# Kernel tuning notes

Hardware: AMD Instinct MI355X
Metric: run time of the kernel (lower is better)

## Reference

```python
import jax, jax.numpy as jnp
import numpy as np

B, H, NC, CS, D = 4, 16, 64, 64, 64
BASE_LR = 1.0
EPS = 1e-6


def setup_inputs() -> dict:
    key = jax.random.key(0)
    ks = jax.random.split(key, 4)
    xk = jax.random.normal(ks[0], (B, H, NC, CS, D), jnp.float32)
    xv = jax.random.normal(ks[1], (B, H, NC, CS, D), jnp.float32)
    # weights/theta use the module's N(0, 0.02) init scale
    weight = 0.02 * jax.random.normal(ks[2], (H, D, D), jnp.float32)
    bias = jnp.zeros((H, 1, D), jnp.float32)
    gamma = jnp.ones((H, 1, D), jnp.float32)
    beta = jnp.zeros((H, 1, D), jnp.float32)
    theta = 0.02 * jax.random.normal(ks[3], (H, D, 1), jnp.float32)
    theta_bias = jnp.zeros((H, 1, 1), jnp.float32)
    alpha = jnp.zeros((CS,), jnp.float32)
    return dict(xk=xk, xv=xv, weight=weight, bias=bias, gamma=gamma,
                beta=beta, theta=theta, theta_bias=theta_bias, alpha=alpha)


def _ttt(xk, xv, weight, bias, gamma, beta, theta, theta_bias, alpha):
    Bq, Hq, NCq, CSq, Dq = xk.shape
    # TTTDynamicLearningGate: token_idx = clamp(1/arange + alpha, 0)
    token_idx = jnp.maximum(1.0 / jnp.arange(1, CSq + 1, dtype=xk.dtype) + alpha, 0.0)
    token_eta = token_idx[None, None, :, None]  # [1,1,CS,1]
    g = gamma[None]       # [1,H,1,D]
    bt = beta[None]       # [1,H,1,D]
    tb = theta_bias[None]  # [1,H,1,1]
    # detach(): tile slow weights over batch -> fast weights
    W0 = jnp.broadcast_to(weight[None], (Bq, Hq, Dq, Dq))
    b0 = jnp.broadcast_to(bias[None], (Bq, Hq, 1, Dq))

    def step(carry, chunk):
        W, b = carry
        xk_c, xv_c = chunk  # [B,H,CS,D]
        # lr gate: eta = token_eta * (base_lr * sigmoid(x @ theta + b) / head_dim)
        lr = jax.nn.sigmoid(jnp.einsum('bhkc,hcd->bhkd', xk_c, theta) + tb)
        eta = token_eta * (BASE_LR * lr / Dq)  # [B,H,CS,1]
        # forward through fast weights (depth = 1)
        z = xk_c @ W + b
        # multi-head LayerNorm, detailed
        mu = z.mean(-1, keepdims=True)
        var = ((z - mu) ** 2).mean(-1, keepdims=True)
        std = jnp.sqrt(var + EPS)
        x_hat = (z - mu) / std
        y = g * x_hat + bt
        # L2 reconstruction grad through LN (manual backward)
        grad_out = y - (xv_c - xk_c)
        gxh = grad_out * g
        grad_x = (Dq * gxh - gxh.sum(-1, keepdims=True)
                  - x_hat * (gxh * x_hat).sum(-1, keepdims=True)) / (Dq * std)
        # fast-weight delta + step()
        dW = jnp.einsum('bhkd,bhke->bhde', eta * xk_c, grad_x)
        db = (eta * grad_x).sum(-2, keepdims=True)
        Wn, bn = W - dW, b - db
        return (Wn, bn), xk_c @ Wn + bn

    chunks = (jnp.moveaxis(xk, 2, 0), jnp.moveaxis(xv, 2, 0))  # [NC,B,H,CS,D]
    (_, _), outs = jax.lax.scan(step, (W0, b0), chunks)
    return jnp.moveaxis(outs, 0, 2)  # [B,H,NC,CS,D]


def reference(xk, xv, weight, bias, gamma, beta, theta, theta_bias, alpha):
    return _ttt(xk, xv, weight, bias, gamma, beta, theta, theta_bias, alpha)
```

## Files before the change

### kernel.cpp

```cpp
#include <hip/hip_runtime.h>
#include <hip/hip_bf16.h>
#include <math.h>

#define NCC 64
#define CSC 64
#define DC 64
#define S 72
#define EPSF 1e-6f
#define LDS_BYTES 66560

typedef __attribute__((ext_vector_type(8))) short bf16x8;
typedef __attribute__((ext_vector_type(4))) float f32x4;
typedef __attribute__((ext_vector_type(4))) short short4v;
typedef __attribute__((ext_vector_type(2))) short short2v;

static __device__ __forceinline__ short cvt_bf16(float x) {
    union { __hip_bfloat16 b; short s; } u;
    u.b = __float2bfloat16(x);
    return u.s;
}
static __device__ __forceinline__ float bf16_to_f(unsigned hw) {
    union { unsigned u; float f; } v; v.u = hw << 16;
    return v.f;
}

#define DPP_ROR_ADD(v, N)                                                     \
    do {                                                                      \
        union { float f; int i; } _u, _r;                                     \
        _u.f = (v);                                                           \
        _r.i = __builtin_amdgcn_mov_dpp(_u.i, 0x120 + (N), 0xF, 0xF, true);   \
        (v) += _r.f;                                                          \
    } while (0)

static __device__ __forceinline__ float red16(float v) {
    DPP_ROR_ADD(v, 1);
    DPP_ROR_ADD(v, 2);
    DPP_ROR_ADD(v, 4);
    DPP_ROR_ADD(v, 8);
    return v;
}

__global__ __launch_bounds__(512, 1) void ttt_kernel(
    const float* __restrict__ xk, const float* __restrict__ xv,
    const float* __restrict__ weight, const float* __restrict__ bias,
    const float* __restrict__ gamma, const float* __restrict__ beta,
    const float* __restrict__ theta, const float* __restrict__ theta_bias,
    const float* __restrict__ alpha, float* __restrict__ out)
{
    extern __shared__ char sb[];
    auto xs_rm = (short (*)[CSC][S])(sb);
    auto xsT   = (short (*)[DC][S]) (sb + 18432);
    auto gsT   = (short (*)[S])     (sb + 36864);
    auto Gr    = (short (*)[S])     (sb + 46080);
    auto Wtb   = (short (*)[S])     (sb + 55296);
    auto dbp   = (float (*)[DC])    (sb + 64512);

    const int t   = threadIdx.x;
    const int w   = t >> 6;
    const bool lo = (w < 4);
    const int ws  = w & 3;
    const int l   = t & 63;
    const int g   = l >> 4, la = l & 15;
    const int r0  = 16*ws + 4*g;
    const int io  = lo ? 0 : 2;
    const int ts  = 64*ws + l;
    const int bh  = blockIdx.x;
    const int h   = bh & 15;

    const size_t bh_off = (size_t)bh * NCC*CSC*DC;
    const float* xkb = xk + bh_off;
    const float* xvb = xv + bh_off;
    float*       ob  = out + bh_off;

    float gam[4], bet[4], thv[4], bcol[4];
#pragma unroll
    for (int n = 0; n < 4; ++n) {
        gam[n]  = gamma[h*DC + 16*n + la];
        bet[n]  = beta [h*DC + 16*n + la];
        thv[n]  = theta[h*DC + 16*n + la];
        bcol[n] = bias [h*DC + 16*n + la];
    }
    const float tb = theta_bias[h];
    float tokk[2];
#pragma unroll
    for (int ii = 0; ii < 2; ++ii) {
        int r = r0 + io + ii;
        tokk[ii] = fmaxf(1.0f/(float)(r+1) + alpha[r], 0.0f);
    }

    float Wreg[4][4];
    float4 xl[4];
    float xkh[4][4];
    float xvg[2][4];

#pragma unroll
    for (int ii = 0; ii < 2; ++ii)
#pragma unroll
        for (int n = 0; n < 4; ++n)
            xvg[ii][n] = xvb[(r0+io+ii)*DC + 16*n + la];

    if (lo) {
        const float* wg = weight + h*DC*DC;
#pragma unroll
        for (int i = 0; i < 4; ++i)
#pragma unroll
            for (int n = 0; n < 4; ++n)
                Wreg[i][n] = wg[(r0+i)*DC + 16*n + la];
#pragma unroll
        for (int n = 0; n < 4; ++n) {
            short4v sv;
#pragma unroll
            for (int i = 0; i < 4; ++i) sv[i] = cvt_bf16(Wreg[i][n]);
            *(short4v*)&Wtb[16*n + la][r0] = sv;
        }
#pragma unroll
        for (int i4 = 0; i4 < 4; ++i4) xl[i4] = ((const float4*)xkb)[ts + 256*i4];
#pragma unroll
        for (int i = 0; i < 4; ++i)
#pragma unroll
            for (int n = 0; n < 4; ++n)
                xkh[i][n] = xkb[(r0+i)*DC + 16*n + la];
#pragma unroll
        for (int i4 = 0; i4 < 4; ++i4) {
            int f = ts + 256*i4, k = f >> 4, j = f & 15;
            short4v s4;
            s4[0]=cvt_bf16(xl[i4].x); s4[1]=cvt_bf16(xl[i4].y);
            s4[2]=cvt_bf16(xl[i4].z); s4[3]=cvt_bf16(xl[i4].w);
            *(short4v*)&xs_rm[0][k][4*j] = s4;
        }
#pragma unroll
        for (int n = 0; n < 4; ++n) {
            short4v sv;
#pragma unroll
            for (int i = 0; i < 4; ++i) sv[i] = cvt_bf16(xkh[i][n]);
            *(short4v*)&xsT[0][16*n + la][r0] = sv;
        }
    }
    __syncthreads();

    for (int c = 0; c < NCC; ++c) {
        const int cb = c & 1, nb = cb ^ 1;
        const bool pf = (c + 1 < NCC);

        const bf16x8 a0 = *(const bf16x8*)&xs_rm[cb][16*ws + la][8*g];
        const bf16x8 a1 = *(const bf16x8*)&xs_rm[cb][16*ws + la][32 + 8*g];
        f32x4 zt[4];
#pragma unroll
        for (int n = 0; n < 4; ++n) {
            bf16x8 w0 = *(const bf16x8*)&Wtb[16*n + la][8*g];
            bf16x8 w1 = *(const bf16x8*)&Wtb[16*n + la][32 + 8*g];
            f32x4 zz = {0.f,0.f,0.f,0.f};
            zz = __builtin_amdgcn_mfma_f32_16x16x32_bf16(a0, w0, zz, 0,0,0);
            zz = __builtin_amdgcn_mfma_f32_16x16x32_bf16(a1, w1, zz, 0,0,0);
            zt[n] = zz;
        }
        if (!lo) {
#pragma unroll
            for (int n = 0; n < 4; ++n) {
                bf16x8 b0 = *(const bf16x8*)&xs_rm[cb][16*n + la][8*g];
                bf16x8 b1 = *(const bf16x8*)&xs_rm[cb][16*n + la][32 + 8*g];
                f32x4 cc = {0.f,0.f,0.f,0.f};
                cc = __builtin_amdgcn_mfma_f32_16x16x32_bf16(a0, b0, cc, 0,0,0);
                cc = __builtin_amdgcn_mfma_f32_16x16x32_bf16(a1, b1, cc, 0,0,0);
                short4v sg;
#pragma unroll
                for (int i = 0; i < 4; ++i) sg[i] = cvt_bf16(cc[i]);
                *(short4v*)&Gr[16*n + la][r0] = sg;
            }
        }

        float xkq[2][4];
#pragma unroll
        for (int n = 0; n < 4; ++n) {
            unsigned pk = *(const unsigned*)&xsT[cb][16*n + la][r0 + io];
            xkq[0][n] = bf16_to_f(pk & 0xFFFFu);
            xkq[1][n] = bf16_to_f(pk >> 16);
        }

        float xvN[2][4];
        if (pf) {
            const float* xvn = xvb + (c+1)*CSC*DC;
#pragma unroll
            for (int ii = 0; ii < 2; ++ii)
#pragma unroll
                for (int n = 0; n < 4; ++n)
                    xvN[ii][n] = xvn[(r0+io+ii)*DC + 16*n + la];
            if (lo) {
                const float* xkn = xkb + (c+1)*CSC*DC;
#pragma unroll
                for (int i4 = 0; i4 < 4; ++i4) xl[i4] = ((const float4*)xkn)[ts + 256*i4];
#pragma unroll
                for (int i = 0; i < 4; ++i)
#pragma unroll
                    for (int n = 0; n < 4; ++n)
                        xkh[i][n] = xkn[(r0+i)*DC + 16*n + la];
            }
        }

        float zrow[2][4];
        if (lo) {
#pragma unroll
            for (int n = 0; n < 4; ++n) { zrow[0][n] = zt[n][0]; zrow[1][n] = zt[n][1]; }
        } else {
#pragma unroll
            for (int n = 0; n < 4; ++n) { zrow[0][n] = zt[n][2]; zrow[1][n] = zt[n][3]; }
        }

        float gsv[2][4];
#pragma unroll
        for (int ii = 0; ii < 2; ++ii) {
            float z4[4];
#pragma unroll
            for (int n = 0; n < 4; ++n) z4[n] = zrow[ii][n] + bcol[n];
            float szz = red16(z4[0]*z4[0] + z4[1]*z4[1] + z4[2]*z4[2] + z4[3]*z4[3]);
            float sz  = red16(z4[0] + z4[1] + z4[2] + z4[3]);
            float thd = red16(xkq[ii][0]*thv[0] + xkq[ii][1]*thv[1] +
                              xkq[ii][2]*thv[2] + xkq[ii][3]*thv[3]);
            float mu   = sz * (1.0f/DC);
            float var  = szz*(1.0f/DC) - mu*mu;
            float rstd = rsqrtf(var + EPSF);
            float ex   = __expf(-(thd + tb));
            float lr   = __builtin_amdgcn_rcpf(1.0f + ex);
            float eta  = tokk[ii]*lr*(1.0f/DC);
            float xh[4], gxh[4], a1v = 0.f, a2v = 0.f;
#pragma unroll
            for (int n = 0; n < 4; ++n) {
                xh[n] = (z4[n]-mu)*rstd;
                float y  = fmaf(gam[n], xh[n], bet[n]);
                float go = y - xvg[ii][n] + xkq[ii][n];
                gxh[n] = go*gam[n];
                a1v += gxh[n];
                a2v = fmaf(gxh[n], xh[n], a2v);
            }
            float s1 = red16(a1v), s2 = red16(a2v);
            float sc = rstd*(1.0f/DC)*eta;
#pragma unroll
            for (int n = 0; n < 4; ++n)
                gsv[ii][n] = (64.f*gxh[n] - s1 - xh[n]*s2)*sc;
        }
#pragma unroll
        for (int n = 0; n < 4; ++n) {
            short2v sg;
            sg[0] = cvt_bf16(gsv[0][n]);
            sg[1] = cvt_bf16(gsv[1][n]);
            *(short2v*)&gsT[16*n + la][r0 + io] = sg;
        }
        float dbl[4];
#pragma unroll
        for (int n = 0; n < 4; ++n) {
            float dd = gsv[0][n] + gsv[1][n];
            dd += __shfl_xor(dd, 16);
            dd += __shfl_xor(dd, 32);
            dbl[n] = dd;
        }
        if (l < 16) {
            f32x4 dv = {dbl[0], dbl[1], dbl[2], dbl[3]};
            *(f32x4*)&dbp[w][4*la] = dv;
        }
        __syncthreads();

        {
            f32x4 s = *(const f32x4*)&dbp[0][4*la];
#pragma unroll
            for (int p = 1; p < 8; ++p) {
                f32x4 d = *(const f32x4*)&dbp[p][4*la];
#pragma unroll
                for (int n = 0; n < 4; ++n) s[n] += d[n];
            }
#pragma unroll
            for (int n = 0; n < 4; ++n) bcol[n] -= s[n];
        }

        if (lo) {
            const bf16x8 ax0 = *(const bf16x8*)&xsT[cb][16*ws + la][8*g];
            const bf16x8 ax1 = *(const bf16x8*)&xsT[cb][16*ws + la][32 + 8*g];
#pragma unroll
            for (int n = 0; n < 4; ++n) {
                bf16x8 q0 = *(const bf16x8*)&gsT[16*n + la][8*g];
                bf16x8 q1 = *(const bf16x8*)&gsT[16*n + la][32 + 8*g];
                f32x4 dw = {0.f,0.f,0.f,0.f};
                dw = __builtin_amdgcn_mfma_f32_16x16x32_bf16(ax0, q0, dw, 0,0,0);
                dw = __builtin_amdgcn_mfma_f32_16x16x32_bf16(ax1, q1, dw, 0,0,0);
                short4v sw;
#pragma unroll
                for (int i = 0; i < 4; ++i) {
                    Wreg[i][n] -= dw[i];
                    sw[i] = cvt_bf16(Wreg[i][n]);
                }
                *(short4v*)&Wtb[16*n + la][r0] = sw;
            }
            if (pf) {
#pragma unroll
                for (int i4 = 0; i4 < 4; ++i4) {
                    int f = ts + 256*i4, k = f >> 4, j = f & 15;
                    short4v s4;
                    s4[0]=cvt_bf16(xl[i4].x); s4[1]=cvt_bf16(xl[i4].y);
                    s4[2]=cvt_bf16(xl[i4].z); s4[3]=cvt_bf16(xl[i4].w);
                    *(short4v*)&xs_rm[nb][k][4*j] = s4;
                }
#pragma unroll
                for (int n = 0; n < 4; ++n) {
                    short4v sv;
#pragma unroll
                    for (int i = 0; i < 4; ++i) sv[i] = cvt_bf16(xkh[i][n]);
                    *(short4v*)&xsT[nb][16*n + la][r0] = sv;
                }
            }
        } else {
            const bf16x8 ar0 = *(const bf16x8*)&Gr[16*ws + la][8*g];
            const bf16x8 ar1 = *(const bf16x8*)&Gr[16*ws + la][32 + 8*g];
            float* oc = ob + c*CSC*DC;
#pragma unroll
            for (int n = 0; n < 4; ++n) {
                bf16x8 q0 = *(const bf16x8*)&gsT[16*n + la][8*g];
                bf16x8 q1 = *(const bf16x8*)&gsT[16*n + la][32 + 8*g];
                f32x4 og = {0.f,0.f,0.f,0.f};
                og = __builtin_amdgcn_mfma_f32_16x16x32_bf16(ar0, q0, og, 0,0,0);
                og = __builtin_amdgcn_mfma_f32_16x16x32_bf16(ar1, q1, og, 0,0,0);
#pragma unroll
                for (int i = 0; i < 4; ++i)
                    oc[(r0+i)*DC + 16*n + la] = zt[n][i] - og[i] + bcol[n];
            }
        }
        if (pf) {
#pragma unroll
            for (int ii = 0; ii < 2; ++ii)
#pragma unroll
                for (int n = 0; n < 4; ++n)
                    xvg[ii][n] = xvN[ii][n];
        }
        __syncthreads();
    }
}

extern "C" void kernel_launch(void* const* d_in, const int* in_sizes, int n_in,
                              void* d_out, int out_size, void* d_ws, size_t ws_size,
                              hipStream_t stream) {
    const float* xk         = (const float*)d_in[0];
    const float* xv         = (const float*)d_in[1];
    const float* weight     = (const float*)d_in[2];
    const float* bias       = (const float*)d_in[3];
    const float* gamma      = (const float*)d_in[4];
    const float* beta       = (const float*)d_in[5];
    const float* theta      = (const float*)d_in[6];
    const float* theta_bias = (const float*)d_in[7];
    const float* alpha      = (const float*)d_in[8];
    float* out = (float*)d_out;

    (void)hipFuncSetAttribute((const void*)ttt_kernel,
                              hipFuncAttributeMaxDynamicSharedMemorySize,
                              LDS_BYTES);
    ttt_kernel<<<64, 512, LDS_BYTES, stream>>>(xk, xv, weight, bias, gamma, beta,
                                               theta, theta_bias, alpha, out);
}
```

Baseline: 145.7 us.

## Split TTT chunk work between wave groups and use 32x32 MFMA tiles

Restructures the per-chunk work split. The low waves now own the full LayerNorm backward for their 16 rows, the weight update and the prefetch. The high waves compute the z forward and the Gram matrix with 32x32x16 MFMA and write the output, so the two groups no longer both run the z MFMA and the LN math. The bias correction is folded into Gr as +1 and the high waves carry their own bias column, which shrinks dbp to four entries and drops the xsT readback. This aims to cut duplicated work and MFMA instruction count, at the cost of more load imbalance between the two wave groups and higher register use on the low waves.

```diff
diff --git a/kernel.cpp b/kernel.cpp
--- a/kernel.cpp
+++ b/kernel.cpp
@@ -7,21 +7,17 @@
 #define DC 64
 #define S 72
 #define EPSF 1e-6f
-#define LDS_BYTES 66560
-
-typedef __attribute__((ext_vector_type(8))) short bf16x8;
-typedef __attribute__((ext_vector_type(4))) float f32x4;
-typedef __attribute__((ext_vector_type(4))) short short4v;
-typedef __attribute__((ext_vector_type(2))) short short2v;
+#define LDS_BYTES 65536
+
+typedef __attribute__((ext_vector_type(8)))  short bf16x8;
+typedef __attribute__((ext_vector_type(4)))  float f32x4;
+typedef __attribute__((ext_vector_type(16))) float f32x16;
+typedef __attribute__((ext_vector_type(4)))  short short4v;
 
 static __device__ __forceinline__ short cvt_bf16(float x) {
     union { __hip_bfloat16 b; short s; } u;
     u.b = __float2bfloat16(x);
     return u.s;
-}
-static __device__ __forceinline__ float bf16_to_f(unsigned hw) {
-    union { unsigned u; float f; } v; v.u = hw << 16;
-    return v.f;
 }
 
 #define DPP_ROR_ADD(v, N)                                                     \
@@ -61,8 +57,9 @@
     const int ws  = w & 3;
     const int l   = t & 63;
     const int g   = l >> 4, la = l & 15;
+    const int la5 = l & 31, hi5 = l >> 5;
+    const int R   = ws >> 1, E = ws & 1;
     const int r0  = 16*ws + 4*g;
-    const int io  = lo ? 0 : 2;
     const int ts  = 64*ws + l;
     const int bh  = blockIdx.x;
     const int h   = bh & 15;
@@ -72,54 +69,46 @@
     const float* xvb = xv + bh_off;
     float*       ob  = out + bh_off;
 
-    float gam[4], bet[4], thv[4], bcol[4];
-#pragma unroll
-    for (int n = 0; n < 4; ++n) {
-        gam[n]  = gamma[h*DC + 16*n + la];
-        bet[n]  = beta [h*DC + 16*n + la];
-        thv[n]  = theta[h*DC + 16*n + la];
-        bcol[n] = bias [h*DC + 16*n + la];
-    }
-    const float tb = theta_bias[h];
-    float tokk[2];
-#pragma unroll
-    for (int ii = 0; ii < 2; ++ii) {
-        int r = r0 + io + ii;
-        tokk[ii] = fmaxf(1.0f/(float)(r+1) + alpha[r], 0.0f);
-    }
-
-    float Wreg[4][4];
+    float gam[4], bet[4], thv[4], tok[4], bcol[4], tb = 0.f;
+    float Wreg[16];
     float4 xl[4];
-    float xkh[4][4];
-    float xvg[2][4];
-
-#pragma unroll
-    for (int ii = 0; ii < 2; ++ii)
-#pragma unroll
-        for (int n = 0; n < 4; ++n)
-            xvg[ii][n] = xvb[(r0+io+ii)*DC + 16*n + la];
+    float xkh[4][4], xkE[4][4], xvg[4][4], xvN[4][4];
+    float bcolh = 0.f;
+    f32x16 z32;
 
     if (lo) {
+#pragma unroll
+        for (int n = 0; n < 4; ++n) {
+            gam[n]  = gamma[h*DC + 16*n + la];
+            bet[n]  = beta [h*DC + 16*n + la];
+            thv[n]  = theta[h*DC + 16*n + la];
+            bcol[n] = bias [h*DC + 16*n + la];
+        }
+        tb = theta_bias[h];
+#pragma unroll
+        for (int i = 0; i < 4; ++i)
+            tok[i] = fmaxf(1.0f/(float)(r0+i+1) + alpha[r0+i], 0.0f);
         const float* wg = weight + h*DC*DC;
 #pragma unroll
+        for (int q = 0; q < 4; ++q) {
+            short4v sw;
+#pragma unroll
+            for (int j = 0; j < 4; ++j) {
+                Wreg[4*q+j] = wg[(32*R + 8*q + 4*hi5 + j)*DC + 32*E + la5];
+                sw[j] = cvt_bf16(Wreg[4*q+j]);
+            }
+            *(short4v*)&Wtb[32*E + la5][32*R + 8*q + 4*hi5] = sw;
+        }
+#pragma unroll
+        for (int i4 = 0; i4 < 4; ++i4) xl[i4] = ((const float4*)xkb)[ts + 256*i4];
+#pragma unroll
         for (int i = 0; i < 4; ++i)
 #pragma unroll
-            for (int n = 0; n < 4; ++n)
-                Wreg[i][n] = wg[(r0+i)*DC + 16*n + la];
-#pragma unroll
-        for (int n = 0; n < 4; ++n) {
-            short4v sv;
-#pragma unroll
-            for (int i = 0; i < 4; ++i) sv[i] = cvt_bf16(Wreg[i][n]);
-            *(short4v*)&Wtb[16*n + la][r0] = sv;
-        }
-#pragma unroll
-        for (int i4 = 0; i4 < 4; ++i4) xl[i4] = ((const float4*)xkb)[ts + 256*i4];
-#pragma unroll
-        for (int i = 0; i < 4; ++i)
-#pragma unroll
-            for (int n = 0; n < 4; ++n)
+            for (int n = 0; n < 4; ++n) {
                 xkh[i][n] = xkb[(r0+i)*DC + 16*n + la];
+                xvg[i][n] = xvb[(r0+i)*DC + 16*n + la];
+                xkE[i][n] = xkh[i][n];
+            }
 #pragma unroll
         for (int i4 = 0; i4 < 4; ++i4) {
             int f = ts + 256*i4, k = f >> 4, j = f & 15;
@@ -135,6 +124,8 @@
             for (int i = 0; i < 4; ++i) sv[i] = cvt_bf16(xkh[i][n]);
             *(short4v*)&xsT[0][16*n + la][r0] = sv;
         }
+    } else {
+        bcolh = bias[h*DC + 32*E + la5];
     }
     __syncthreads();
 
@@ -142,152 +133,141 @@
         const int cb = c & 1, nb = cb ^ 1;
         const bool pf = (c + 1 < NCC);
 
-        const bf16x8 a0 = *(const bf16x8*)&xs_rm[cb][16*ws + la][8*g];
-        const bf16x8 a1 = *(const bf16x8*)&xs_rm[cb][16*ws + la][32 + 8*g];
-        f32x4 zt[4];
-#pragma unroll
-        for (int n = 0; n < 4; ++n) {
-            bf16x8 w0 = *(const bf16x8*)&Wtb[16*n + la][8*g];
-            bf16x8 w1 = *(const bf16x8*)&Wtb[16*n + la][32 + 8*g];
-            f32x4 zz = {0.f,0.f,0.f,0.f};
-            zz = __builtin_amdgcn_mfma_f32_16x16x32_bf16(a0, w0, zz, 0,0,0);
-            zz = __builtin_amdgcn_mfma_f32_16x16x32_bf16(a1, w1, zz, 0,0,0);
-            zt[n] = zz;
-        }
-        if (!lo) {
+        if (lo) {
+            const bf16x8 a0 = *(const bf16x8*)&xs_rm[cb][16*ws + la][8*g];
+            const bf16x8 a1 = *(const bf16x8*)&xs_rm[cb][16*ws + la][32 + 8*g];
+            f32x4 zt[4];
 #pragma unroll
             for (int n = 0; n < 4; ++n) {
-                bf16x8 b0 = *(const bf16x8*)&xs_rm[cb][16*n + la][8*g];
-                bf16x8 b1 = *(const bf16x8*)&xs_rm[cb][16*n + la][32 + 8*g];
-                f32x4 cc = {0.f,0.f,0.f,0.f};
-                cc = __builtin_amdgcn_mfma_f32_16x16x32_bf16(a0, b0, cc, 0,0,0);
-                cc = __builtin_amdgcn_mfma_f32_16x16x32_bf16(a1, b1, cc, 0,0,0);
+                bf16x8 w0 = *(const bf16x8*)&Wtb[16*n + la][8*g];
+                bf16x8 w1 = *(const bf16x8*)&Wtb[16*n + la][32 + 8*g];
+                f32x4 zz = {0.f,0.f,0.f,0.f};
+                zz = __builtin_amdgcn_mfma_f32_16x16x32_bf16(a0, w0, zz, 0,0,0);
+                zz = __builtin_amdgcn_mfma_f32_16x16x32_bf16(a1, w1, zz, 0,0,0);
+                zt[n] = zz;
+            }
+            if (pf) {
+                const float* xkn = xkb + (c+1)*CSC*DC;
+                const float* xvn = xvb + (c+1)*CSC*DC;
+#pragma unroll
+                for (int i4 = 0; i4 < 4; ++i4) xl[i4] = ((const float4*)xkn)[ts + 256*i4];
+#pragma unroll
+                for (int i = 0; i < 4; ++i)
+#pragma unroll
+                    for (int n = 0; n < 4; ++n) {
+                        xkh[i][n] = xkn[(r0+i)*DC + 16*n + la];
+                        xvN[i][n] = xvn[(r0+i)*DC + 16*n + la];
+                    }
+            }
+            float gsv[4][4];
+#pragma unroll
+            for (int i = 0; i < 4; ++i) {
+                float z0 = zt[0][i]+bcol[0], z1 = zt[1][i]+bcol[1];
+                float z2 = zt[2][i]+bcol[2], z3 = zt[3][i]+bcol[3];
+                float szz = red16(z0*z0 + z1*z1 + z2*z2 + z3*z3);
+                float sz  = red16(z0 + z1 + z2 + z3);
+                float thd = red16(xkE[i][0]*thv[0] + xkE[i][1]*thv[1] +
+                                  xkE[i][2]*thv[2] + xkE[i][3]*thv[3]);
+                float mu   = sz * (1.0f/DC);
+                float var  = szz*(1.0f/DC) - mu*mu;
+                float rstd = rsqrtf(var + EPSF);
+                float ex   = __expf(-(thd + tb));
+                float lr   = __builtin_amdgcn_rcpf(1.0f + ex);
+                float eta  = tok[i]*lr*(1.0f/DC);
+                float zz4[4] = {z0,z1,z2,z3};
+                float xh[4], gxh[4], a1v = 0.f, a2v = 0.f;
+#pragma unroll
+                for (int n = 0; n < 4; ++n) {
+                    xh[n] = (zz4[n]-mu)*rstd;
+                    float y  = fmaf(gam[n], xh[n], bet[n]);
+                    float go = y - xvg[i][n] + xkE[i][n];
+                    gxh[n] = go*gam[n];
+                    a1v += gxh[n];
+                    a2v = fmaf(gxh[n], xh[n], a2v);
+                }
+                float s1 = red16(a1v), s2 = red16(a2v);
+                float sc = rstd*(1.0f/DC)*eta;
+#pragma unroll
+                for (int n = 0; n < 4; ++n)
+                    gsv[i][n] = (64.f*gxh[n] - s1 - xh[n]*s2)*sc;
+            }
+#pragma unroll
+            for (int n = 0; n < 4; ++n) {
                 short4v sg;
 #pragma unroll
-                for (int i = 0; i < 4; ++i) sg[i] = cvt_bf16(cc[i]);
-                *(short4v*)&Gr[16*n + la][r0] = sg;
-            }
-        }
-
-        float xkq[2][4];
-#pragma unroll
-        for (int n = 0; n < 4; ++n) {
-            unsigned pk = *(const unsigned*)&xsT[cb][16*n + la][r0 + io];
-            xkq[0][n] = bf16_to_f(pk & 0xFFFFu);
-            xkq[1][n] = bf16_to_f(pk >> 16);
-        }
-
-        float xvN[2][4];
-        if (pf) {
-            const float* xvn = xvb + (c+1)*CSC*DC;
-#pragma unroll
-            for (int ii = 0; ii < 2; ++ii)
-#pragma unroll
-                for (int n = 0; n < 4; ++n)
-                    xvN[ii][n] = xvn[(r0+io+ii)*DC + 16*n + la];
-            if (lo) {
-                const float* xkn = xkb + (c+1)*CSC*DC;
-#pragma unroll
-                for (int i4 = 0; i4 < 4; ++i4) xl[i4] = ((const float4*)xkn)[ts + 256*i4];
-#pragma unroll
-                for (int i = 0; i < 4; ++i)
-#pragma unroll
-                    for (int n = 0; n < 4; ++n)
-                        xkh[i][n] = xkn[(r0+i)*DC + 16*n + la];
-            }
-        }
-
-        float zrow[2][4];
+                for (int i = 0; i < 4; ++i) sg[i] = cvt_bf16(gsv[i][n]);
+                *(short4v*)&gsT[16*n + la][r0] = sg;
+            }
+            float dbl[4];
+#pragma unroll
+            for (int n = 0; n < 4; ++n) {
+                float dd = gsv[0][n]+gsv[1][n]+gsv[2][n]+gsv[3][n];
+                dd += __shfl_xor(dd, 16);
+                dd += __shfl_xor(dd, 32);
+                dbl[n] = dd;
+            }
+            if (l < 16) {
+                f32x4 dv = {dbl[0], dbl[1], dbl[2], dbl[3]};
+                *(f32x4*)&dbp[ws][4*la] = dv;
+            }
+        } else {
+            bf16x8 az[4], bz[4];
+#pragma unroll
+            for (int s = 0; s < 4; ++s) {
+                az[s] = *(const bf16x8*)&xs_rm[cb][32*R + la5][16*s + 8*hi5];
+                bz[s] = *(const bf16x8*)&Wtb[32*E + la5][16*s + 8*hi5];
+            }
+            f32x16 zz = {0.f,0.f,0.f,0.f,0.f,0.f,0.f,0.f,
+                         0.f,0.f,0.f,0.f,0.f,0.f,0.f,0.f};
+#pragma unroll
+            for (int s = 0; s < 4; ++s)
+                zz = __builtin_amdgcn_mfma_f32_32x32x16_bf16(az[s], bz[s], zz, 0,0,0);
+            z32 = zz;
+            bf16x8 bg[4];
+            if (R == E) {
+#pragma unroll
+                for (int s = 0; s < 4; ++s) bg[s] = az[s];
+            } else {
+#pragma unroll
+                for (int s = 0; s < 4; ++s)
+                    bg[s] = *(const bf16x8*)&xs_rm[cb][32*E + la5][16*s + 8*hi5];
+            }
+            f32x16 gg = {0.f,0.f,0.f,0.f,0.f,0.f,0.f,0.f,
+                         0.f,0.f,0.f,0.f,0.f,0.f,0.f,0.f};
+#pragma unroll
+            for (int s = 0; s < 4; ++s)
+                gg = __builtin_amdgcn_mfma_f32_32x32x16_bf16(az[s], bg[s], gg, 0,0,0);
+#pragma unroll
+            for (int q = 0; q < 4; ++q) {
+                short4v sg;
+#pragma unroll
+                for (int j = 0; j < 4; ++j) sg[j] = cvt_bf16(gg[4*q+j] + 1.0f);
+                *(short4v*)&Gr[32*E + la5][32*R + 8*q + 4*hi5] = sg;
+            }
+        }
+        __syncthreads();
+
         if (lo) {
-#pragma unroll
-            for (int n = 0; n < 4; ++n) { zrow[0][n] = zt[n][0]; zrow[1][n] = zt[n][1]; }
-        } else {
-#pragma unroll
-            for (int n = 0; n < 4; ++n) { zrow[0][n] = zt[n][2]; zrow[1][n] = zt[n][3]; }
-        }
-
-        float gsv[2][4];
-#pragma unroll
-        for (int ii = 0; ii < 2; ++ii) {
-            float z4[4];
-#pragma unroll
-            for (int n = 0; n < 4; ++n) z4[n] = zrow[ii][n] + bcol[n];
-            float szz = red16(z4[0]*z4[0] + z4[1]*z4[1] + z4[2]*z4[2] + z4[3]*z4[3]);
-            float sz  = red16(z4[0] + z4[1] + z4[2] + z4[3]);
-            float thd = red16(xkq[ii][0]*thv[0] + xkq[ii][1]*thv[1] +
-                              xkq[ii][2]*thv[2] + xkq[ii][3]*thv[3]);
-            float mu   = sz * (1.0f/DC);
-            float var  = szz*(1.0f/DC) - mu*mu;
-            float rstd = rsqrtf(var + EPSF);
-            float ex   = __expf(-(thd + tb));
-            float lr   = __builtin_amdgcn_rcpf(1.0f + ex);
-            float eta  = tokk[ii]*lr*(1.0f/DC);
-            float xh[4], gxh[4], a1v = 0.f, a2v = 0.f;
-#pragma unroll
-            for (int n = 0; n < 4; ++n) {
-                xh[n] = (z4[n]-mu)*rstd;
-                float y  = fmaf(gam[n], xh[n], bet[n]);
-                float go = y - xvg[ii][n] + xkq[ii][n];
-                gxh[n] = go*gam[n];
-                a1v += gxh[n];
-                a2v = fmaf(gxh[n], xh[n], a2v);
-            }
-            float s1 = red16(a1v), s2 = red16(a2v);
-            float sc = rstd*(1.0f/DC)*eta;
-#pragma unroll
-            for (int n = 0; n < 4; ++n)
-                gsv[ii][n] = (64.f*gxh[n] - s1 - xh[n]*s2)*sc;
-        }
-#pragma unroll
-        for (int n = 0; n < 4; ++n) {
-            short2v sg;
-            sg[0] = cvt_bf16(gsv[0][n]);
-            sg[1] = cvt_bf16(gsv[1][n]);
-            *(short2v*)&gsT[16*n + la][r0 + io] = sg;
-        }
-        float dbl[4];
-#pragma unroll
-        for (int n = 0; n < 4; ++n) {
-            float dd = gsv[0][n] + gsv[1][n];
-            dd += __shfl_xor(dd, 16);
-            dd += __shfl_xor(dd, 32);
-            dbl[n] = dd;
-        }
-        if (l < 16) {
-            f32x4 dv = {dbl[0], dbl[1], dbl[2], dbl[3]};
-            *(f32x4*)&dbp[w][4*la] = dv;
-        }
-        __syncthreads();
-
-        {
-            f32x4 s = *(const f32x4*)&dbp[0][4*la];
-#pragma unroll
-            for (int p = 1; p < 8; ++p) {
-                f32x4 d = *(const f32x4*)&dbp[p][4*la];
-#pragma unroll
-                for (int n = 0; n < 4; ++n) s[n] += d[n];
-            }
-#pragma unroll
-            for (int n = 0; n < 4; ++n) bcol[n] -= s[n];
-        }
-
-        if (lo) {
-            const bf16x8 ax0 = *(const bf16x8*)&xsT[cb][16*ws + la][8*g];
-            const bf16x8 ax1 = *(const bf16x8*)&xsT[cb][16*ws + la][32 + 8*g];
-#pragma unroll
-            for (int n = 0; n < 4; ++n) {
-                bf16x8 q0 = *(const bf16x8*)&gsT[16*n + la][8*g];
-                bf16x8 q1 = *(const bf16x8*)&gsT[16*n + la][32 + 8*g];
-                f32x4 dw = {0.f,0.f,0.f,0.f};
-                dw = __builtin_amdgcn_mfma_f32_16x16x32_bf16(ax0, q0, dw, 0,0,0);
-                dw = __builtin_amdgcn_mfma_f32_16x16x32_bf16(ax1, q1, dw, 0,0,0);
+            bf16x8 ax[4], bx[4];
+#pragma unroll
+            for (int s = 0; s < 4; ++s) {
+                ax[s] = *(const bf16x8*)&xsT[cb][32*R + la5][16*s + 8*hi5];
+                bx[s] = *(const bf16x8*)&gsT[32*E + la5][16*s + 8*hi5];
+            }
+            f32x16 dw = {0.f,0.f,0.f,0.f,0.f,0.f,0.f,0.f,
+                         0.f,0.f,0.f,0.f,0.f,0.f,0.f,0.f};
+#pragma unroll
+            for (int s = 0; s < 4; ++s)
+                dw = __builtin_amdgcn_mfma_f32_32x32x16_bf16(ax[s], bx[s], dw, 0,0,0);
+#pragma unroll
+            for (int q = 0; q < 4; ++q) {
                 short4v sw;
 #pragma unroll
-                for (int i = 0; i < 4; ++i) {
-                    Wreg[i][n] -= dw[i];
-                    sw[i] = cvt_bf16(Wreg[i][n]);
-                }
-                *(short4v*)&Wtb[16*n + la][r0] = sw;
+                for (int j = 0; j < 4; ++j) {
+                    Wreg[4*q+j] -= dw[4*q+j];
+                    sw[j] = cvt_bf16(Wreg[4*q+j]);
+                }
+                *(short4v*)&Wtb[32*E + la5][32*R + 8*q + 4*hi5] = sw;
             }
             if (pf) {
 #pragma unroll
@@ -305,29 +285,54 @@
                     for (int i = 0; i < 4; ++i) sv[i] = cvt_bf16(xkh[i][n]);
                     *(short4v*)&xsT[nb][16*n + la][r0] = sv;
                 }
+#pragma unroll
+                for (int i = 0; i < 4; ++i)
+#pragma unroll
+                    for (int n = 0; n < 4; ++n) {
+                        xkE[i][n] = xkh[i][n];
+                        xvg[i][n] = xvN[i][n];
+                    }
+            }
+            {
+                f32x4 s = *(const f32x4*)&dbp[0][4*la];
+#pragma unroll
+                for (int p = 1; p < 4; ++p) {
+                    f32x4 d = *(const f32x4*)&dbp[p][4*la];
+#pragma unroll
+                    for (int n = 0; n < 4; ++n) s[n] += d[n];
+                }
+#pragma unroll
+                for (int n = 0; n < 4; ++n) bcol[n] -= s[n];
             }
         } else {
-            const bf16x8 ar0 = *(const bf16x8*)&Gr[16*ws + la][8*g];
-            const bf16x8 ar1 = *(const bf16x8*)&Gr[16*ws + la][32 + 8*g];
+            bf16x8 ag[4], bq[4];
+#pragma unroll
+            for (int s = 0; s < 4; ++s) {
+                ag[s] = *(const bf16x8*)&Gr[32*R + la5][16*s + 8*hi5];
+                bq[s] = *(const bf16x8*)&gsT[32*E + la5][16*s + 8*hi5];
+            }
+            f32x16 og = {0.f,0.f,0.f,0.f,0.f,0.f,0.f,0.f,
+                         0.f,0.f,0.f,0.f,0.f,0.f,0.f,0.f};
+#pragma unroll
+            for (int s = 0; s < 4; ++s)
+                og = __builtin_amdgcn_mfma_f32_32x32x16_bf16(ag[s], bq[s], og, 0,0,0);
             float* oc = ob + c*CSC*DC;
 #pragma unroll
-            for (int n = 0; n < 4; ++n) {
-                bf16x8 q0 = *(const bf16x8*)&gsT[16*n + la][8*g];
-                bf16x8 q1 = *(const bf16x8*)&gsT[16*n + la][32 + 8*g];
-                f32x4 og = {0.f,0.f,0.f,0.f};
-                og = __builtin_amdgcn_mfma_f32_16x16x32_bf16(ar0, q0, og, 0,0,0);
-                og = __builtin_amdgcn_mfma_f32_16x16x32_bf16(ar1, q1, og, 0,0,0);
-#pragma unroll
-                for (int i = 0; i < 4; ++i)
-                    oc[(r0+i)*DC + 16*n + la] = zt[n][i] - og[i] + bcol[n];
-            }
-        }
-        if (pf) {
-#pragma unroll
-            for (int ii = 0; ii < 2; ++ii)
-#pragma unroll
-                for (int n = 0; n < 4; ++n)
-                    xvg[ii][n] = xvN[ii][n];
+            for (int q = 0; q < 4; ++q)
+#pragma unroll
+                for (int j = 0; j < 4; ++j) {
+                    int r = 4*q + j;
+                    oc[(32*R + 8*q + 4*hi5 + j)*DC + 32*E + la5] =
+                        z32[r] - og[r] + bcolh;
+                }
+            {
+                int idx = 4*(la5 & 15) + 2*E + (la5 >> 4);
+                float s0 = dbp[0][idx];
+                s0 += dbp[1][idx];
+                s0 += dbp[2][idx];
+                s0 += dbp[3][idx];
+                bcolh -= s0;
+            }
         }
         __syncthreads();
     }
```

After: 157.7 us. +8.2%, slower.

## Stage chunk outputs in LDS for coalesced deferred stores; fold bias delta into Gram matmul

Applied to the files above, without the earlier changes.

Each chunk's output tile is now written transposed into an LDS buffer. All eight waves store it to global memory with float4 writes at the start of the next iteration, and the last chunk is flushed after the loop. This replaces the scattered per-lane scalar stores and lets the write overlap the next chunk's compute. The bias is kept in LDS and updated by a single wave. The bias-gradient term is folded into the output matmul by adding 1 to the bf16 Gram entries, which removes the per-thread reduction over all waves. This costs extra LDS, an added sync dependency on the output buffer, and a small precision change from rounding G+1 to bf16.

```diff
diff --git a/kernel.cpp b/kernel.cpp
--- a/kernel.cpp
+++ b/kernel.cpp
@@ -6,8 +6,9 @@
 #define CSC 64
 #define DC 64
 #define S 72
+#define SO 68
 #define EPSF 1e-6f
-#define LDS_BYTES 66560
+#define LDS_BYTES 84224
 
 typedef __attribute__((ext_vector_type(8))) short bf16x8;
 typedef __attribute__((ext_vector_type(4))) float f32x4;
@@ -54,6 +55,8 @@
     auto Gr    = (short (*)[S])     (sb + 46080);
     auto Wtb   = (short (*)[S])     (sb + 55296);
     auto dbp   = (float (*)[DC])    (sb + 64512);
+    auto outb  = (float (*)[SO])    (sb + 66560);
+    auto bs    = (float*)           (sb + 83968);
 
     const int t   = threadIdx.x;
     const int w   = t >> 6;
@@ -72,13 +75,12 @@
     const float* xvb = xv + bh_off;
     float*       ob  = out + bh_off;
 
-    float gam[4], bet[4], thv[4], bcol[4];
+    float gam[4], bet[4], thv[4];
 #pragma unroll
     for (int n = 0; n < 4; ++n) {
-        gam[n]  = gamma[h*DC + 16*n + la];
-        bet[n]  = beta [h*DC + 16*n + la];
-        thv[n]  = theta[h*DC + 16*n + la];
-        bcol[n] = bias [h*DC + 16*n + la];
+        gam[n] = gamma[h*DC + 16*n + la];
+        bet[n] = beta [h*DC + 16*n + la];
+        thv[n] = theta[h*DC + 16*n + la];
     }
     const float tb = theta_bias[h];
     float tokk[2];
@@ -87,6 +89,8 @@
         int r = r0 + io + ii;
         tokk[ii] = fmaxf(1.0f/(float)(r+1) + alpha[r], 0.0f);
     }
+
+    if (t < DC) bs[t] = bias[h*DC + 16*(t & 3) + (t >> 2)];
 
     float Wreg[4][4];
     float4 xl[4];
@@ -141,6 +145,21 @@
     for (int c = 0; c < NCC; ++c) {
         const int cb = c & 1, nb = cb ^ 1;
         const bool pf = (c + 1 < NCC);
+
+        f32x4 bold = *(const f32x4*)&bs[4*la];
+        if (c > 0) {
+            float* ocp = ob + (c-1)*CSC*DC;
+            const int kk = 4*w + (l >> 4);
+            const int e0 = 4*(l & 15);
+#pragma unroll
+            for (int p = 0; p < 2; ++p) {
+                int k2 = kk + 32*p;
+                float4 v;
+                v.x = outb[e0+0][k2]; v.y = outb[e0+1][k2];
+                v.z = outb[e0+2][k2]; v.w = outb[e0+3][k2];
+                *(float4*)(ocp + k2*DC + e0) = v;
+            }
+        }
 
         const bf16x8 a0 = *(const bf16x8*)&xs_rm[cb][16*ws + la][8*g];
         const bf16x8 a1 = *(const bf16x8*)&xs_rm[cb][16*ws + la][32 + 8*g];
@@ -164,7 +183,7 @@
                 cc = __builtin_amdgcn_mfma_f32_16x16x32_bf16(a1, b1, cc, 0,0,0);
                 short4v sg;
 #pragma unroll
-                for (int i = 0; i < 4; ++i) sg[i] = cvt_bf16(cc[i]);
+                for (int i = 0; i < 4; ++i) sg[i] = cvt_bf16(cc[i] + 1.0f);
                 *(short4v*)&Gr[16*n + la][r0] = sg;
             }
         }
@@ -211,7 +230,7 @@
         for (int ii = 0; ii < 2; ++ii) {
             float z4[4];
 #pragma unroll
-            for (int n = 0; n < 4; ++n) z4[n] = zrow[ii][n] + bcol[n];
+            for (int n = 0; n < 4; ++n) z4[n] = zrow[ii][n] + bold[n];
             float szz = red16(z4[0]*z4[0] + z4[1]*z4[1] + z4[2]*z4[2] + z4[3]*z4[3]);
             float sz  = red16(z4[0] + z4[1] + z4[2] + z4[3]);
             float thd = red16(xkq[ii][0]*thv[0] + xkq[ii][1]*thv[1] +
@@ -259,18 +278,6 @@
         }
         __syncthreads();
 
-        {
-            f32x4 s = *(const f32x4*)&dbp[0][4*la];
-#pragma unroll
-            for (int p = 1; p < 8; ++p) {
-                f32x4 d = *(const f32x4*)&dbp[p][4*la];
-#pragma unroll
-                for (int n = 0; n < 4; ++n) s[n] += d[n];
-            }
-#pragma unroll
-            for (int n = 0; n < 4; ++n) bcol[n] -= s[n];
-        }
-
         if (lo) {
             const bf16x8 ax0 = *(const bf16x8*)&xsT[cb][16*ws + la][8*g];
             const bf16x8 ax1 = *(const bf16x8*)&xsT[cb][16*ws + la][32 + 8*g];
@@ -306,10 +313,15 @@
                     *(short4v*)&xsT[nb][16*n + la][r0] = sv;
                 }
             }
+            if (w == 0) {
+                float s = dbp[0][l];
+#pragma unroll
+                for (int p = 1; p < 8; ++p) s += dbp[p][l];
+                bs[l] -= s;
+            }
         } else {
             const bf16x8 ar0 = *(const bf16x8*)&Gr[16*ws + la][8*g];
             const bf16x8 ar1 = *(const bf16x8*)&Gr[16*ws + la][32 + 8*g];
-            float* oc = ob + c*CSC*DC;
 #pragma unroll
             for (int n = 0; n < 4; ++n) {
                 bf16x8 q0 = *(const bf16x8*)&gsT[16*n + la][8*g];
@@ -317,9 +329,11 @@
                 f32x4 og = {0.f,0.f,0.f,0.f};
                 og = __builtin_amdgcn_mfma_f32_16x16x32_bf16(ar0, q0, og, 0,0,0);
                 og = __builtin_amdgcn_mfma_f32_16x16x32_bf16(ar1, q1, og, 0,0,0);
+                f32x4 ov;
 #pragma unroll
                 for (int i = 0; i < 4; ++i)
-                    oc[(r0+i)*DC + 16*n + la] = zt[n][i] - og[i] + bcol[n];
+                    ov[i] = zt[n][i] - og[i] + bold[n];
+                *(f32x4*)&outb[16*n + la][r0] = ov;
             }
         }
         if (pf) {
@@ -330,6 +344,20 @@
                     xvg[ii][n] = xvN[ii][n];
         }
         __syncthreads();
+    }
+
+    {
+        float* ocp = ob + (NCC-1)*CSC*DC;
+        const int kk = 4*w + (l >> 4);
+        const int e0 = 4*(l & 15);
+#pragma unroll
+        for (int p = 0; p < 2; ++p) {
+            int k2 = kk + 32*p;
+            float4 v;
+            v.x = outb[e0+0][k2]; v.y = outb[e0+1][k2];
+            v.z = outb[e0+2][k2]; v.w = outb[e0+3][k2];
+            *(float4*)(ocp + k2*DC + e0) = v;
+        }
     }
 }
 
```

Measured after the change: 179.7 us. 23.4% more time.
